# Optimization experiments

Measured on AMD Instinct MI355X. Metric: run time of the kernel, lower is better.

## Reference

```python
import jax, jax.numpy as jnp
import numpy as np

NF4_LEVELS = jnp.array([-1.0, -0.6962, -0.5251, -0.3949, -0.2844, -0.1848, -0.0911, 0.0,
                        0.0796, 0.1609, 0.2461, 0.3379, 0.4407, 0.5626, 0.723, 1.0], dtype=jnp.float32)
OUT_FEATURES = 4096
IN_FEATURES = 4096
BLOCK_SIZE = 1024
NUM_BLOCKS = OUT_FEATURES * IN_FEATURES // BLOCK_SIZE  # 16384

def setup_inputs() -> dict:
    key = jax.random.key(0)
    k1, k2, k3 = jax.random.split(key, 3)
    x = jax.random.normal(k1, (4, 2048, IN_FEATURES), dtype=jnp.float32)
    quant_indices = jax.random.randint(k2, (NUM_BLOCKS, BLOCK_SIZE), 0, 16, dtype=jnp.int32)
    scales = jax.random.uniform(k3, (NUM_BLOCKS,), dtype=jnp.float32)
    return {"x": x, "quant_indices": quant_indices, "scales": scales}

def reference(x, quant_indices, scales):
    # Block-wise NF4 dequantization: levels lookup * per-block absmax scale
    deq = NF4_LEVELS[quant_indices] * scales[:, None]          # [num_blocks, block_size]
    W = deq.reshape(OUT_FEATURES, IN_FEATURES)                 # [out, in]
    # F.linear(x, W): y = x @ W.T
    return jnp.einsum('bsi,oi->bso', x, W)
```

## Files before the change

### kernel.cpp

```cpp
#include <hip/hip_runtime.h>

typedef unsigned short u16;
typedef __attribute__((ext_vector_type(4))) float  f32x4;
typedef __attribute__((ext_vector_type(4))) int    i32x4;
typedef __attribute__((ext_vector_type(4))) unsigned u32x4;
typedef __attribute__((ext_vector_type(8))) short  shortx8;

__device__ __constant__ float NF4C[16] = {
    -1.0f, -0.6962f, -0.5251f, -0.3949f, -0.2844f, -0.1848f, -0.0911f, 0.0f,
     0.0796f, 0.1609f, 0.2461f, 0.3379f, 0.4407f, 0.5626f, 0.723f, 1.0f};

__device__ __forceinline__ unsigned f2bf(float f) {
    unsigned u = __float_as_uint(f);
    return (u + 0x7FFFu + ((u >> 16) & 1u)) >> 16;
}

__device__ __forceinline__ void ld_lds16(const u16* g, u16* l) {
    __builtin_amdgcn_global_load_lds(
        (const __attribute__((address_space(1))) void*)g,
        (__attribute__((address_space(3))) void*)l,
        16, 0, 0);
}


__global__ __launch_bounds__(256) void prep(const float* __restrict__ x,
                                            const int* __restrict__ qi,
                                            const float* __restrict__ sc,
                                            u16* __restrict__ xb,
                                            u16* __restrict__ wb) {
    const size_t nthr = (size_t)gridDim.x * 256;
    const size_t tid  = (size_t)blockIdx.x * 256 + threadIdx.x;

    for (size_t c = tid; c < (33554432u / 8); c += nthr) {
        const size_t i = c * 8;
        f32x4 f0 = __builtin_nontemporal_load((const f32x4*)(x + i));
        f32x4 f1 = __builtin_nontemporal_load((const f32x4*)(x + i + 4));
        u32x4 o;
        o[0] = f2bf(f0[0]) | (f2bf(f0[1]) << 16);
        o[1] = f2bf(f0[2]) | (f2bf(f0[3]) << 16);
        o[2] = f2bf(f1[0]) | (f2bf(f1[1]) << 16);
        o[3] = f2bf(f1[2]) | (f2bf(f1[3]) << 16);
        *(u32x4*)(xb + i) = o;
    }
    for (size_t c = tid; c < (16777216u / 8); c += nthr) {
        const size_t i = c * 8;
        const float s = sc[i >> 10];
        i32x4 q0 = __builtin_nontemporal_load((const i32x4*)(qi + i));
        i32x4 q1 = __builtin_nontemporal_load((const i32x4*)(qi + i + 4));
        u32x4 o;
        o[0] = f2bf(NF4C[q0[0]] * s) | (f2bf(NF4C[q0[1]] * s) << 16);
        o[1] = f2bf(NF4C[q0[2]] * s) | (f2bf(NF4C[q0[3]] * s) << 16);
        o[2] = f2bf(NF4C[q1[0]] * s) | (f2bf(NF4C[q1[1]] * s) << 16);
        o[3] = f2bf(NF4C[q1[2]] * s) | (f2bf(NF4C[q1[3]] * s) << 16);
        *(u32x4*)(wb + i) = o;
    }
}


#define BM 256
#define BN 256
#define BK 64

template<int MODE>
__device__ __forceinline__ void kgroup(
    const u16* __restrict__ Ar, const u16* __restrict__ Br,
    u16* dA1, u16* dB1,
    u16* dBc,
    const u16* gA1, const u16* gB1,
    int wm, int wn, int r16, int c0, int c1,
    f32x4 (&acc)[8][4])
{
    constexpr size_t K = 4096;
    shortx8 a[4], a2[4], b[4];

#pragma unroll
    for (int j = 0; j < 4; j++)
        b[j] = *(const shortx8*)&Br[(wn + j * 16 + r16) * 64 + c0 * 8];
#pragma unroll
    for (int i = 0; i < 4; i++)
        a[i] = *(const shortx8*)&Ar[(wm + i * 16 + r16) * 64 + c0 * 8];
    if constexpr (MODE <= 1) {
        ld_lds16(gB1 + 128 * K, dB1 + 128 * 64);
        ld_lds16(gB1 + 192 * K, dB1 + 192 * 64);
    }
    __builtin_amdgcn_s_setprio(1);
#pragma unroll
    for (int i = 0; i < 4; i++)
#pragma unroll
        for (int j = 0; j < 4; j++)
            acc[i][j] = __builtin_amdgcn_mfma_f32_16x16x32_bf16(a[i], b[j], acc[i][j], 0, 0, 0);
    __builtin_amdgcn_s_setprio(0);

#pragma unroll
    for (int i = 0; i < 4; i++)
        a2[i] = *(const shortx8*)&Ar[(wm + 64 + i * 16 + r16) * 64 + c0 * 8];
    if constexpr (MODE <= 1) {
        ld_lds16(gA1,           dA1);
        ld_lds16(gA1 + 128 * K, dA1 + 128 * 64);
    }
    __builtin_amdgcn_s_setprio(1);
#pragma unroll
    for (int i = 0; i < 4; i++)
#pragma unroll
        for (int j = 0; j < 4; j++)
            acc[4 + i][j] = __builtin_amdgcn_mfma_f32_16x16x32_bf16(a2[i], b[j], acc[4 + i][j], 0, 0, 0);
    __builtin_amdgcn_s_setprio(0);

#pragma unroll
    for (int j = 0; j < 4; j++)
        b[j] = *(const shortx8*)&Br[(wn + j * 16 + r16) * 64 + c1 * 8];
#pragma unroll
    for (int i = 0; i < 4; i++)
        a[i] = *(const shortx8*)&Ar[(wm + i * 16 + r16) * 64 + c1 * 8];
    if constexpr (MODE <= 1) {
        ld_lds16(gA1 +  64 * K, dA1 +  64 * 64);
        ld_lds16(gA1 + 192 * K, dA1 + 192 * 64);
    }
    __builtin_amdgcn_s_setprio(1);
#pragma unroll
    for (int i = 0; i < 4; i++)
#pragma unroll
        for (int j = 0; j < 4; j++)
            acc[i][j] = __builtin_amdgcn_mfma_f32_16x16x32_bf16(a[i], b[j], acc[i][j], 0, 0, 0);
    __builtin_amdgcn_s_setprio(0);
    if constexpr (MODE == 0)
        asm volatile("s_barrier" ::: "memory");

#pragma unroll
    for (int i = 0; i < 4; i++)
        a2[i] = *(const shortx8*)&Ar[(wm + 64 + i * 16 + r16) * 64 + c1 * 8];
    if constexpr (MODE == 0) {
        ld_lds16(gB1 + 64,          dBc);
        ld_lds16(gB1 + 64 + 64 * K, dBc + 64 * 64);
    }
    __builtin_amdgcn_s_setprio(1);
#pragma unroll
    for (int i = 0; i < 4; i++)
#pragma unroll
        for (int j = 0; j < 4; j++)
            acc[4 + i][j] = __builtin_amdgcn_mfma_f32_16x16x32_bf16(a2[i], b[j], acc[4 + i][j], 0, 0, 0);
    __builtin_amdgcn_s_setprio(0);
    if constexpr (MODE == 0) {
        asm volatile("s_waitcnt vmcnt(2)" ::: "memory");
        asm volatile("s_barrier" ::: "memory");
    } else if constexpr (MODE == 1) {
        asm volatile("s_waitcnt vmcnt(0)" ::: "memory");
        asm volatile("s_barrier" ::: "memory");
    }
}

__global__ __launch_bounds__(512, 2) void gemm_bt(const u16* __restrict__ A,
                                                  const u16* __restrict__ B,
                                                  float* __restrict__ C) {
    constexpr size_t K = 4096;
    constexpr int N = 4096;
    __shared__ __align__(16) u16 As[2][BM * BK];
    __shared__ __align__(16) u16 Bs[2][BN * BK];

    const int t    = threadIdx.x;
    const int wave = t >> 6;
    const int lane = t & 63;
    const int quad = lane >> 4;
    const int r16  = lane & 15;

    const int id  = blockIdx.x;
    const int xcd = id & 7;
    const int loc = id >> 3;
    const int bm  = (xcd * 4 + (loc >> 4)) * BM;
    const int bn  = (loc & 15) * BN;

    const int lrow = (wave << 3) + (lane >> 3);
    const int lch  = (lane & 7) ^ (lane >> 3);
    const u16* sA = A + (size_t)(bm + lrow) * K + lch * 8;
    const u16* sB = B + (size_t)(bn + lrow) * K + lch * 8;

    const int w512 = wave * 512;
    u16* dA0 = &As[0][w512];  u16* dA1 = &As[1][w512];
    u16* dB0 = &Bs[0][w512];  u16* dB1 = &Bs[1][w512];

    const int wm = (wave >> 2) * 128;
    const int wn = (wave & 3) * 64;
    const int c0 = quad ^ (r16 & 7);
    const int c1 = c0 ^ 4;

    f32x4 acc[8][4];
#pragma unroll
    for (int i = 0; i < 8; i++)
#pragma unroll
        for (int j = 0; j < 4; j++) acc[i][j] = (f32x4)0.0f;

#pragma unroll
    for (int r0 = 0; r0 < 256; r0 += 64) {
        ld_lds16(sA + (size_t)r0 * K, dA0 + r0 * 64);
        ld_lds16(sB + (size_t)r0 * K, dB0 + r0 * 64);
    }
    ld_lds16(sB + 64,                  dB1);
    ld_lds16(sB + 64 + (size_t)64 * K, dB1 + 64 * 64);
    asm volatile("s_waitcnt vmcnt(2)" ::: "memory");
    asm volatile("s_barrier" ::: "memory");

    const u16* gA1 = sA + 64;
    const u16* gB1 = sB + 64;
#pragma unroll 1
    for (int u = 0; u < 62; u += 2) {
        kgroup<0>(As[0], Bs[0], dA1, dB1, dB0, gA1, gB1, wm, wn, r16, c0, c1, acc);
        gA1 += 64; gB1 += 64;
        kgroup<0>(As[1], Bs[1], dA0, dB0, dB1, gA1, gB1, wm, wn, r16, c0, c1, acc);
        gA1 += 64; gB1 += 64;
    }
    kgroup<1>(As[0], Bs[0], dA1, dB1, dB0, gA1, gB1, wm, wn, r16, c0, c1, acc);
    kgroup<2>(As[1], Bs[1], dA0, dB0, dB1, gA1, gB1, wm, wn, r16, c0, c1, acc);

#pragma unroll
    for (int i = 0; i < 8; i++) {
        const int row0 = bm + wm + i * 16 + quad * 4;
#pragma unroll
        for (int j = 0; j < 4; j++) {
            const int col = bn + wn + j * 16 + r16;
            float* cp = &C[(size_t)row0 * N + col];
#pragma unroll
            for (int v = 0; v < 4; ++v)
                cp[(size_t)v * N] = acc[i][j][v];
        }
    }
}


__global__ __launch_bounds__(256) void fallback_gemm(const float* __restrict__ x,
                                                     const int* __restrict__ qi,
                                                     const float* __restrict__ sc,
                                                     float* __restrict__ y) {
    __shared__ float xs[16][16];
    __shared__ float wsm[16][17];
    const int tx = threadIdx.x, ty = threadIdx.y;
    const int m = blockIdx.y * 16 + ty;
    const int nrow = blockIdx.x * 16 + ty;
    float acc = 0.f;
    for (int k0 = 0; k0 < 4096; k0 += 16) {
        xs[ty][tx] = x[(size_t)m * 4096 + k0 + tx];
        const size_t fi = (size_t)nrow * 4096 + k0 + tx;
        wsm[ty][tx] = NF4C[qi[fi]] * sc[fi >> 10];
        __syncthreads();
#pragma unroll
        for (int kk = 0; kk < 16; kk++) acc += xs[ty][kk] * wsm[tx][kk];
        __syncthreads();
    }
    y[(size_t)m * 4096 + blockIdx.x * 16 + tx] = acc;
}


extern "C" void kernel_launch(void* const* d_in, const int* in_sizes, int n_in,
                              void* d_out, int out_size, void* d_ws, size_t ws_size,
                              hipStream_t stream) {
    const float* x  = (const float*)d_in[0];
    const int*   qi = (const int*)d_in[1];
    const float* sc = (const float*)d_in[2];
    float* y = (float*)d_out;

    const int M = 8192, N = 4096, K = 4096;
    const size_t xb_bytes = (size_t)M * K * 2;
    const size_t wb_bytes = (size_t)N * K * 2;

    if (ws_size >= xb_bytes + wb_bytes) {
        u16* xb = (u16*)d_ws;
        u16* wb = (u16*)((char*)d_ws + xb_bytes);
        prep<<<2048, 256, 0, stream>>>(x, qi, sc, xb, wb);
        gemm_bt<<<(M / BM) * (N / BN), 512, 0, stream>>>(xb, wb, y);
    } else {
        dim3 block(16, 16);
        dim3 grid(N / 16, M / 16);
        fallback_gemm<<<grid, block, 0, stream>>>(x, qi, sc, y);
    }
}
```

Measured before the change: 478.3 us.

## Load B fragments directly from global into registers, dropping B shared-memory staging

The B (dequantized weight) tile is no longer staged through LDS. Each wave now reads its B MFMA fragments straight from global memory into registers, with one k-step of register prefetch. LDS then holds only the A double buffer, which removes the B LDS writes and reads and halves shared-memory use. In exchange, B fragment loads are uncoalesced, and each wave re-fetches B rows that other waves in the block also read, which adds global and L2 traffic and register pressure.

```diff
diff --git a/kernel.cpp b/kernel.cpp
--- a/kernel.cpp
+++ b/kernel.cpp
@@ -61,90 +61,88 @@
 #define BN 256
 #define BK 64
 
+__device__ __forceinline__ f32x4 mfma16(shortx8 a, shortx8 b, f32x4 c) {
+    return __builtin_amdgcn_mfma_f32_16x16x32_bf16(a, b, c, 0, 0, 0);
+}
+
 template<int MODE>
-__device__ __forceinline__ void kgroup(
-    const u16* __restrict__ Ar, const u16* __restrict__ Br,
-    u16* dA1, u16* dB1,
-    u16* dBc,
-    const u16* gA1, const u16* gB1,
-    int wm, int wn, int r16, int c0, int c1,
+__device__ __forceinline__ void ktile(
+    const u16* __restrict__ Ar,
+    u16* dA,
+    const u16* gA,
+    const u16** pb,
+    shortx8 (&b0)[4], shortx8 (&b1)[4],
+    int wm, int r16, int c0, int c1,
     f32x4 (&acc)[8][4])
 {
     constexpr size_t K = 4096;
-    shortx8 a[4], a2[4], b[4];
-
+    shortx8 a[4];
+
+    if constexpr (MODE == 0) {
+        ld_lds16(gA,                  dA);
+        ld_lds16(gA + (size_t)64*K,   dA + 64*64);
+        ld_lds16(gA + (size_t)128*K,  dA + 128*64);
+        ld_lds16(gA + (size_t)192*K,  dA + 192*64);
+    }
 #pragma unroll
     for (int j = 0; j < 4; j++)
-        b[j] = *(const shortx8*)&Br[(wn + j * 16 + r16) * 64 + c0 * 8];
-#pragma unroll
-    for (int i = 0; i < 4; i++)
-        a[i] = *(const shortx8*)&Ar[(wm + i * 16 + r16) * 64 + c0 * 8];
-    if constexpr (MODE <= 1) {
-        ld_lds16(gB1 + 128 * K, dB1 + 128 * 64);
-        ld_lds16(gB1 + 192 * K, dB1 + 192 * 64);
-    }
-    __builtin_amdgcn_s_setprio(1);
-#pragma unroll
-    for (int i = 0; i < 4; i++)
-#pragma unroll
-        for (int j = 0; j < 4; j++)
-            acc[i][j] = __builtin_amdgcn_mfma_f32_16x16x32_bf16(a[i], b[j], acc[i][j], 0, 0, 0);
-    __builtin_amdgcn_s_setprio(0);
-
-#pragma unroll
-    for (int i = 0; i < 4; i++)
-        a2[i] = *(const shortx8*)&Ar[(wm + 64 + i * 16 + r16) * 64 + c0 * 8];
-    if constexpr (MODE <= 1) {
-        ld_lds16(gA1,           dA1);
-        ld_lds16(gA1 + 128 * K, dA1 + 128 * 64);
-    }
-    __builtin_amdgcn_s_setprio(1);
-#pragma unroll
-    for (int i = 0; i < 4; i++)
-#pragma unroll
-        for (int j = 0; j < 4; j++)
-            acc[4 + i][j] = __builtin_amdgcn_mfma_f32_16x16x32_bf16(a2[i], b[j], acc[4 + i][j], 0, 0, 0);
-    __builtin_amdgcn_s_setprio(0);
-
-#pragma unroll
-    for (int j = 0; j < 4; j++)
-        b[j] = *(const shortx8*)&Br[(wn + j * 16 + r16) * 64 + c1 * 8];
-#pragma unroll
-    for (int i = 0; i < 4; i++)
-        a[i] = *(const shortx8*)&Ar[(wm + i * 16 + r16) * 64 + c1 * 8];
-    if constexpr (MODE <= 1) {
-        ld_lds16(gA1 +  64 * K, dA1 +  64 * 64);
-        ld_lds16(gA1 + 192 * K, dA1 + 192 * 64);
-    }
-    __builtin_amdgcn_s_setprio(1);
-#pragma unroll
-    for (int i = 0; i < 4; i++)
-#pragma unroll
-        for (int j = 0; j < 4; j++)
-            acc[i][j] = __builtin_amdgcn_mfma_f32_16x16x32_bf16(a[i], b[j], acc[i][j], 0, 0, 0);
-    __builtin_amdgcn_s_setprio(0);
-    if constexpr (MODE == 0)
-        asm volatile("s_barrier" ::: "memory");
-
-#pragma unroll
-    for (int i = 0; i < 4; i++)
-        a2[i] = *(const shortx8*)&Ar[(wm + 64 + i * 16 + r16) * 64 + c1 * 8];
+        b1[j] = *(const shortx8*)(pb[j] + 32);
+    __builtin_amdgcn_sched_barrier(0x78F);
+
+#pragma unroll
+    for (int i = 0; i < 4; i++)
+        a[i] = *(const shortx8*)&Ar[(wm + i*16 + r16) * 64 + c0 * 8];
+    __builtin_amdgcn_s_setprio(1);
+#pragma unroll
+    for (int i = 0; i < 4; i++)
+#pragma unroll
+        for (int j = 0; j < 4; j++)
+            acc[i][j] = mfma16(a[i], b0[j], acc[i][j]);
+    __builtin_amdgcn_s_setprio(0);
+
+#pragma unroll
+    for (int i = 0; i < 4; i++)
+        a[i] = *(const shortx8*)&Ar[(wm + 64 + i*16 + r16) * 64 + c0 * 8];
+    __builtin_amdgcn_s_setprio(1);
+#pragma unroll
+    for (int i = 0; i < 4; i++)
+#pragma unroll
+        for (int j = 0; j < 4; j++)
+            acc[4 + i][j] = mfma16(a[i], b0[j], acc[4 + i][j]);
+    __builtin_amdgcn_s_setprio(0);
+
     if constexpr (MODE == 0) {
-        ld_lds16(gB1 + 64,          dBc);
-        ld_lds16(gB1 + 64 + 64 * K, dBc + 64 * 64);
-    }
-    __builtin_amdgcn_s_setprio(1);
-#pragma unroll
-    for (int i = 0; i < 4; i++)
-#pragma unroll
-        for (int j = 0; j < 4; j++)
-            acc[4 + i][j] = __builtin_amdgcn_mfma_f32_16x16x32_bf16(a2[i], b[j], acc[4 + i][j], 0, 0, 0);
-    __builtin_amdgcn_s_setprio(0);
+#pragma unroll
+        for (int j = 0; j < 4; j++) {
+            pb[j] += 64;
+            b0[j] = *(const shortx8*)pb[j];
+        }
+    }
+
+#pragma unroll
+    for (int i = 0; i < 4; i++)
+        a[i] = *(const shortx8*)&Ar[(wm + i*16 + r16) * 64 + c1 * 8];
+    __builtin_amdgcn_s_setprio(1);
+#pragma unroll
+    for (int i = 0; i < 4; i++)
+#pragma unroll
+        for (int j = 0; j < 4; j++)
+            acc[i][j] = mfma16(a[i], b1[j], acc[i][j]);
+    __builtin_amdgcn_s_setprio(0);
+
+#pragma unroll
+    for (int i = 0; i < 4; i++)
+        a[i] = *(const shortx8*)&Ar[(wm + 64 + i*16 + r16) * 64 + c1 * 8];
+    __builtin_amdgcn_s_setprio(1);
+#pragma unroll
+    for (int i = 0; i < 4; i++)
+#pragma unroll
+        for (int j = 0; j < 4; j++)
+            acc[4 + i][j] = mfma16(a[i], b1[j], acc[4 + i][j]);
+    __builtin_amdgcn_s_setprio(0);
+
     if constexpr (MODE == 0) {
-        asm volatile("s_waitcnt vmcnt(2)" ::: "memory");
-        asm volatile("s_barrier" ::: "memory");
-    } else if constexpr (MODE == 1) {
-        asm volatile("s_waitcnt vmcnt(0)" ::: "memory");
+        asm volatile("s_waitcnt vmcnt(4)" ::: "memory");
         asm volatile("s_barrier" ::: "memory");
     }
 }
@@ -155,7 +153,6 @@
     constexpr size_t K = 4096;
     constexpr int N = 4096;
     __shared__ __align__(16) u16 As[2][BM * BK];
-    __shared__ __align__(16) u16 Bs[2][BN * BK];
 
     const int t    = threadIdx.x;
     const int wave = t >> 6;
@@ -172,44 +169,46 @@
     const int lrow = (wave << 3) + (lane >> 3);
     const int lch  = (lane & 7) ^ (lane >> 3);
     const u16* sA = A + (size_t)(bm + lrow) * K + lch * 8;
-    const u16* sB = B + (size_t)(bn + lrow) * K + lch * 8;
 
     const int w512 = wave * 512;
-    u16* dA0 = &As[0][w512];  u16* dA1 = &As[1][w512];
-    u16* dB0 = &Bs[0][w512];  u16* dB1 = &Bs[1][w512];
+    u16* dA0 = &As[0][w512];
+    u16* dA1 = &As[1][w512];
 
     const int wm = (wave >> 2) * 128;
     const int wn = (wave & 3) * 64;
     const int c0 = quad ^ (r16 & 7);
     const int c1 = c0 ^ 4;
 
+    const u16* pb[4];
+#pragma unroll
+    for (int j = 0; j < 4; j++)
+        pb[j] = B + (size_t)(bn + wn + j * 16 + r16) * K + quad * 8;
+
     f32x4 acc[8][4];
 #pragma unroll
     for (int i = 0; i < 8; i++)
 #pragma unroll
         for (int j = 0; j < 4; j++) acc[i][j] = (f32x4)0.0f;
 
-#pragma unroll
-    for (int r0 = 0; r0 < 256; r0 += 64) {
-        ld_lds16(sA + (size_t)r0 * K, dA0 + r0 * 64);
-        ld_lds16(sB + (size_t)r0 * K, dB0 + r0 * 64);
-    }
-    ld_lds16(sB + 64,                  dB1);
-    ld_lds16(sB + 64 + (size_t)64 * K, dB1 + 64 * 64);
-    asm volatile("s_waitcnt vmcnt(2)" ::: "memory");
+    shortx8 b0[4], b1[4];
+
+    ld_lds16(sA,                  dA0);
+    ld_lds16(sA + (size_t)64*K,   dA0 + 64*64);
+    ld_lds16(sA + (size_t)128*K,  dA0 + 128*64);
+    ld_lds16(sA + (size_t)192*K,  dA0 + 192*64);
+#pragma unroll
+    for (int j = 0; j < 4; j++) b0[j] = *(const shortx8*)pb[j];
+    asm volatile("s_waitcnt vmcnt(4)" ::: "memory");
     asm volatile("s_barrier" ::: "memory");
 
-    const u16* gA1 = sA + 64;
-    const u16* gB1 = sB + 64;
+    const u16* gA = sA + 64;
 #pragma unroll 1
     for (int u = 0; u < 62; u += 2) {
-        kgroup<0>(As[0], Bs[0], dA1, dB1, dB0, gA1, gB1, wm, wn, r16, c0, c1, acc);
-        gA1 += 64; gB1 += 64;
-        kgroup<0>(As[1], Bs[1], dA0, dB0, dB1, gA1, gB1, wm, wn, r16, c0, c1, acc);
-        gA1 += 64; gB1 += 64;
-    }
-    kgroup<1>(As[0], Bs[0], dA1, dB1, dB0, gA1, gB1, wm, wn, r16, c0, c1, acc);
-    kgroup<2>(As[1], Bs[1], dA0, dB0, dB1, gA1, gB1, wm, wn, r16, c0, c1, acc);
+        ktile<0>(As[0], dA1, gA, pb, b0, b1, wm, r16, c0, c1, acc); gA += 64;
+        ktile<0>(As[1], dA0, gA, pb, b0, b1, wm, r16, c0, c1, acc); gA += 64;
+    }
+    ktile<0>(As[0], dA1, gA, pb, b0, b1, wm, r16, c0, c1, acc);
+    ktile<1>(As[1], nullptr, nullptr, pb, b0, b1, wm, r16, c0, c1, acc);
 
 #pragma unroll
     for (int i = 0; i < 8; i++) {
```

After: 530.1 us. 1.11x slower.
